# Performance work log

Measured on AMD Instinct MI355X. Metric: run time of the kernel, lower is better.

## Reference

```python
import jax, jax.numpy as jnp
import numpy as np

B, T, D, H = 64, 512, 1024, 1024

def setup_inputs() -> dict:
    key = jax.random.key(0)
    ks = jax.random.split(key, 7)
    s = 1.0 / np.sqrt(H).astype(np.float32)
    return {
        "x": jax.random.normal(ks[0], (B, T, D), jnp.float32),
        "hidden_state": jax.random.normal(ks[1], (1, B, H), jnp.float32),
        "dones": jax.random.randint(ks[2], (B, T), 0, 2, jnp.int32),
        "W_ih": jax.random.normal(ks[3], (3 * H, D), jnp.float32) * s,
        "W_hh": jax.random.normal(ks[4], (3 * H, H), jnp.float32) * s,
        "b_ih": jax.random.normal(ks[5], (3 * H,), jnp.float32) * s,
        "b_hh": jax.random.normal(ks[6], (3 * H,), jnp.float32) * s,
    }

def _resetting_gru(x, h0, dones, W_ih, W_hh, b_ih, b_hh):
    # x: [B,T,D], h0: [1,B,H], dones: [B,T]
    # Precompute input projection once: [B,T,3H] -> time-major [T,B,3H]
    gi = jnp.einsum('btd,gd->btg', x, W_ih) + b_ih
    gi = jnp.swapaxes(gi, 0, 1)
    # mask[t,b] = 0 where done==1 (hidden zeroed before consuming step t)
    mask = (1.0 - dones.astype(x.dtype)).T[:, :, None]  # [T,B,1]

    def step(h, inp):
        gi_t, m_t = inp          # [B,3H], [B,1]
        h = h * m_t              # inline reset at done timesteps
        gh = h @ W_hh.T + b_hh   # [B,3H]
        ir, iz, in_ = jnp.split(gi_t, 3, axis=-1)
        hr, hz, hn = jnp.split(gh, 3, axis=-1)
        r = jax.nn.sigmoid(ir + hr)
        z = jax.nn.sigmoid(iz + hz)
        n = jnp.tanh(in_ + r * hn)
        h_new = (1.0 - z) * n + z * h
        return h_new, h_new

    h_last, outs = jax.lax.scan(step, h0[0], (gi, mask))
    return jnp.swapaxes(outs, 0, 1), h_last[None]  # [B,T,H], [1,B,H]

def reference(x, hidden_state, dones, W_ih, W_hh, b_ih, b_hh):
    return _resetting_gru(x, hidden_state, dones, W_ih, W_hh, b_ih, b_hh)
```

## Files before the change

### kernel.cpp

```cpp
#include <hip/hip_runtime.h>
#include <hip/hip_cooperative_groups.h>

typedef short s16x8 __attribute__((ext_vector_type(8)));
typedef float f32x4 __attribute__((ext_vector_type(4)));
typedef float f32x2 __attribute__((ext_vector_type(2)));
typedef unsigned int u32x4 __attribute__((ext_vector_type(4)));
typedef unsigned int u32x2 __attribute__((ext_vector_type(2)));

#define B_ 64
#define T_ 512
#define D_ 1024
#define H_ 1024
#define TC_ 128

__device__ __forceinline__ unsigned short f2bf(float f) {
  union { float f; unsigned int u; } v; v.f = f;
  unsigned int r = v.u + 0x7fffu + ((v.u >> 16) & 1u);
  return (unsigned short)(r >> 16);
}
__device__ __forceinline__ float bf2f(unsigned short h) {
  union { unsigned int u; float f; } v; v.u = ((unsigned int)h) << 16;
  return v.f;
}

__device__ __forceinline__ void g2l16(const unsigned short* g, unsigned short* l) {
  __builtin_amdgcn_global_load_lds((const __attribute__((address_space(1))) unsigned int*)g,
                                   (__attribute__((address_space(3))) unsigned int*)l, 16, 0, 0);
}

__device__ __forceinline__ int haddr(int b, int k) {
  return (((b >> 4) * 32 + (k >> 5)) << 9) + ((b & 15) << 5) + (k & 31);
}

__global__ __launch_bounds__(256) void k_cvt_w(const float* __restrict__ w1, unsigned short* __restrict__ o1,
                                               const float* __restrict__ w2, unsigned short* __restrict__ o2) {
  int i = (blockIdx.x * 256 + threadIdx.x) * 4;
  float4 a = *(const float4*)(w1 + i);
  u32x2 p;
  p.x = (unsigned)f2bf(a.x) | ((unsigned)f2bf(a.y) << 16);
  p.y = (unsigned)f2bf(a.z) | ((unsigned)f2bf(a.w) << 16);
  *(u32x2*)(o1 + i) = p;
  float4 b = *(const float4*)(w2 + i);
  u32x2 q;
  q.x = (unsigned)f2bf(b.x) | ((unsigned)f2bf(b.y) << 16);
  q.y = (unsigned)f2bf(b.z) | ((unsigned)f2bf(b.w) << 16);
  *(u32x2*)(o2 + i) = q;
}

__global__ __launch_bounds__(256) void k_xt(const float* __restrict__ x, unsigned short* __restrict__ xt, int t0) {
  int m = blockIdx.x;
  int t = t0 + (m >> 6), b = m & 63;
  const float* src = x + ((size_t)(b * T_ + t)) * D_;
  unsigned short* dst = xt + (size_t)m * D_;
  int d = threadIdx.x * 4;
  float4 a = *(const float4*)(src + d);
  u32x2 p;
  p.x = (unsigned)f2bf(a.x) | ((unsigned)f2bf(a.y) << 16);
  p.y = (unsigned)f2bf(a.z) | ((unsigned)f2bf(a.w) << 16);
  *(u32x2*)(dst + d) = p;
}

__global__ __launch_bounds__(256) void k_misc(const float* __restrict__ h0, const int* __restrict__ dones,
                                              unsigned short* __restrict__ hb16T, float* __restrict__ hchk,
                                              float* __restrict__ maskT, unsigned int* __restrict__ bar,
                                              unsigned int* __restrict__ flag) {
  int i = blockIdx.x * 256 + threadIdx.x;
  int b = i >> 10, k = i & 1023;
  float v = h0[i];
  hchk[i] = v;
  int m0 = dones[b * T_];
  hb16T[haddr(b, k)] = m0 ? (unsigned short)0 : f2bf(v);
  if (i < T_ * B_) {
    int t = i >> 6, bb = i & 63;
    maskT[i] = dones[bb * T_ + t] ? 0.f : 1.f;
  }
  if (i == 0) { *bar = 0u; *flag = 0u; }
}

__global__ __launch_bounds__(256) void k_gemm(const unsigned short* __restrict__ A,
                                              const unsigned short* __restrict__ Bm,
                                              const float* __restrict__ bias,
                                              unsigned short* __restrict__ C) {
  __shared__ __align__(16) unsigned short As[128 * 40];
  __shared__ __align__(16) unsigned short Bs[128 * 40];
  const int tid = threadIdx.x;
  const int wave = tid >> 6, lane = tid & 63;
  const int q = lane >> 4, r = lane & 15;
  const int wm = wave >> 1, wn = wave & 1;
  const long m0 = (long)blockIdx.y * 128, n0 = (long)blockIdx.x * 128;
  f32x4 acc[4][4] = {};
  for (int k0 = 0; k0 < 1024; k0 += 32) {
    __syncthreads();
#pragma unroll
    for (int c0 = 0; c0 < 2; ++c0) {
      int c = c0 * 256 + tid;
      int row = c >> 2, kof = (c & 3) * 8;
      *(u32x4*)&As[row * 40 + kof] = *(const u32x4*)(A + (m0 + row) * 1024 + k0 + kof);
      *(u32x4*)&Bs[row * 40 + kof] = *(const u32x4*)(Bm + (n0 + row) * 1024 + k0 + kof);
    }
    __syncthreads();
    s16x8 af[4], bfr[4];
#pragma unroll
    for (int mt = 0; mt < 4; ++mt)
      af[mt] = *(const s16x8*)&As[(wm * 64 + mt * 16 + r) * 40 + q * 8];
#pragma unroll
    for (int nt = 0; nt < 4; ++nt)
      bfr[nt] = *(const s16x8*)&Bs[(wn * 64 + nt * 16 + r) * 40 + q * 8];
#pragma unroll
    for (int mt = 0; mt < 4; ++mt)
#pragma unroll
      for (int nt = 0; nt < 4; ++nt)
        acc[mt][nt] = __builtin_amdgcn_mfma_f32_16x16x32_bf16(af[mt], bfr[nt], acc[mt][nt], 0, 0, 0);
  }
#pragma unroll
  for (int nt = 0; nt < 4; ++nt) {
    long n = n0 + wn * 64 + nt * 16 + r;
    float bn = bias[n];
#pragma unroll
    for (int mt = 0; mt < 4; ++mt) {
#pragma unroll
      for (int reg = 0; reg < 4; ++reg) {
        long m = m0 + wm * 64 + mt * 16 + q * 4 + reg;
        C[m * 3072 + n] = f2bf(acc[mt][nt][reg] + bn);
      }
    }
  }
}

__global__ __launch_bounds__(512, 2) void k_gru(const unsigned short* __restrict__ whh,
                                                const float* __restrict__ bhh,
                                                const unsigned short* __restrict__ gi,
                                                const float* __restrict__ maskT,
                                                unsigned short* __restrict__ hb16T,
                                                float* __restrict__ hchk,
                                                float* __restrict__ out,
                                                unsigned int* __restrict__ bar,
                                                unsigned int* __restrict__ flag,
                                                int t0) {
  __shared__ __align__(16) unsigned char smem[131072];
  unsigned short* lds_h = (unsigned short*)smem;
  float* red = (float*)smem;
  const int tid = threadIdx.x;
  const int w = tid >> 6, lane = tid & 63;
  const int q = lane >> 4, r = lane & 15;
  const int j0 = blockIdx.x * 16;
  float* hlast = out + (size_t)B_ * T_ * H_;

  s16x8 Wreg[3][4];
#pragma unroll
  for (int g = 0; g < 3; ++g)
#pragma unroll
    for (int ks = 0; ks < 4; ++ks)
      Wreg[g][ks] = *(const s16x8*)(whh + ((size_t)(g * 1024 + j0 + r)) * 1024 + w * 128 + ks * 32 + q * 8);

  const int b0 = w * 8 + q * 2;
  const float bh0 = bhh[j0 + r];
  const float bh1 = bhh[1024 + j0 + r];
  const float bh2 = bhh[2048 + j0 + r];
  float hreg[2];
  hreg[0] = hchk[(size_t)b0 * 1024 + j0 + r];
  hreg[1] = hchk[(size_t)(b0 + 1) * 1024 + j0 + r];

  f32x4 acc[3][4] = {};
  float gcur[6], gnxt[6], mcur[2], mnxt[2], mncur[2], mnnxt[2];
#pragma unroll
  for (int e = 0; e < 2; ++e) {
    size_t mrow = (size_t)(b0 + e) * 3072;
    gcur[e * 3 + 0] = bf2f(gi[mrow + j0 + r]);
    gcur[e * 3 + 1] = bf2f(gi[mrow + 1024 + j0 + r]);
    gcur[e * 3 + 2] = bf2f(gi[mrow + 2048 + j0 + r]);
    mcur[e] = maskT[t0 * 64 + b0 + e];
    int tn = (t0 + 1 < 512) ? t0 + 1 : 511;
    mncur[e] = maskT[tn * 64 + b0 + e];
  }

  for (int tl = 0; tl < TC_; ++tl) {
    const int t = t0 + tl;
    const unsigned short* hsT = hb16T + (size_t)(t & 1) * 65536;
    unsigned short* hdT = hb16T + (size_t)((t + 1) & 1) * 65536;

    for (int c = w; c < 128; c += 8)
      g2l16(hsT + c * 512 + lane * 8, lds_h + c * 512);
    __syncthreads();

#pragma unroll
    for (int ks = 0; ks < 4; ++ks) {
      s16x8 a[4];
#pragma unroll
      for (int bt = 0; bt < 4; ++bt)
        a[bt] = *(const s16x8*)&lds_h[((bt * 32 + w * 4 + ks) << 9) + r * 32 + q * 8];
#pragma unroll
      for (int g = 0; g < 3; ++g)
#pragma unroll
        for (int bt = 0; bt < 4; ++bt)
          acc[g][bt] = __builtin_amdgcn_mfma_f32_16x16x32_bf16(a[bt], Wreg[g][ks], acc[g][bt], 0, 0, 0);
    }
    __syncthreads();

#pragma unroll
    for (int g = 0; g < 3; ++g)
#pragma unroll
      for (int bt = 0; bt < 4; ++bt) {
        *(f32x4*)&red[(size_t)((g * 8 + w) * 16 + r) * 68 + bt * 16 + q * 4] = acc[g][bt];
        acc[g][bt] = (f32x4){0.f, 0.f, 0.f, 0.f};
      }
    __syncthreads();

    f32x2 ps[3];
#pragma unroll
    for (int g = 0; g < 3; ++g) {
      f32x2 s = {0.f, 0.f};
#pragma unroll
      for (int kp = 0; kp < 8; ++kp)
        s += *(const f32x2*)&red[(size_t)((g * 8 + kp) * 16 + r) * 68 + b0];
      ps[g] = s;
    }
    float hn2[2];
#pragma unroll
    for (int e = 0; e < 2; ++e) {
      int b = b0 + e;
      float ghr = ps[0][e] + bh0;
      float ghz = ps[1][e] + bh1;
      float ghn = ps[2][e] + bh2;
      float rr = 1.f / (1.f + __expf(-(gcur[e * 3 + 0] + ghr)));
      float zz = 1.f / (1.f + __expf(-(gcur[e * 3 + 1] + ghz)));
      float nn = tanhf(gcur[e * 3 + 2] + rr * ghn);
      float hp = hreg[e] * mcur[e];
      float hn = (1.f - zz) * nn + zz * hp;
      hreg[e] = hn;
      hn2[e] = hn;
      unsigned short hv = (mncur[e] == 0.f) ? (unsigned short)0 : f2bf(hn);
      hdT[haddr(b, j0 + r)] = hv;
    }
    __syncthreads();

    if (tid == 0) {
      unsigned tgt = (unsigned)(t + 1);
      unsigned old = __hip_atomic_fetch_add(bar, 1u, __ATOMIC_RELEASE, __HIP_MEMORY_SCOPE_AGENT);
      if (old == 64u * tgt - 1u)
        __hip_atomic_store(flag, tgt, __ATOMIC_RELEASE, __HIP_MEMORY_SCOPE_AGENT);
    }

#pragma unroll
    for (int e = 0; e < 2; ++e) {
      int b = b0 + e;
      out[((size_t)b * 512 + t) * 1024 + j0 + r] = hn2[e];
      if (t == 511) hlast[(size_t)b * 1024 + j0 + r] = hn2[e];
      if (tl == TC_ - 1) hchk[(size_t)b * 1024 + j0 + r] = hn2[e];
    }
    if (tl + 1 < TC_) {
#pragma unroll
      for (int e = 0; e < 2; ++e) {
        size_t mrow = (size_t)((tl + 1) * 64 + b0 + e) * 3072;
        gnxt[e * 3 + 0] = bf2f(gi[mrow + j0 + r]);
        gnxt[e * 3 + 1] = bf2f(gi[mrow + 1024 + j0 + r]);
        gnxt[e * 3 + 2] = bf2f(gi[mrow + 2048 + j0 + r]);
        mnxt[e] = maskT[(t + 1) * 64 + b0 + e];
        int tn = (t + 2 < 512) ? t + 2 : 511;
        mnnxt[e] = maskT[tn * 64 + b0 + e];
      }
    }

    if (tid == 0) {
      while (__hip_atomic_load(flag, __ATOMIC_RELAXED, __HIP_MEMORY_SCOPE_AGENT) < (unsigned)(t + 1))
        __builtin_amdgcn_s_sleep(1);
      (void)__hip_atomic_load(bar, __ATOMIC_ACQUIRE, __HIP_MEMORY_SCOPE_AGENT);
    }
    __syncthreads();

#pragma unroll
    for (int e = 0; e < 2; ++e) {
      gcur[e * 3 + 0] = gnxt[e * 3 + 0];
      gcur[e * 3 + 1] = gnxt[e * 3 + 1];
      gcur[e * 3 + 2] = gnxt[e * 3 + 2];
      mcur[e] = mnxt[e];
      mncur[e] = mnnxt[e];
    }
  }
}

extern "C" void kernel_launch(void* const* d_in, const int* in_sizes, int n_in,
                              void* d_out, int out_size, void* d_ws, size_t ws_size,
                              hipStream_t stream) {
  const float* x     = (const float*)d_in[0];
  const float* h0    = (const float*)d_in[1];
  const int*   dones = (const int*)d_in[2];
  const float* Wih   = (const float*)d_in[3];
  const float* Whh   = (const float*)d_in[4];
  const float* bih   = (const float*)d_in[5];
  const float* bhh   = (const float*)d_in[6];
  float* out = (float*)d_out;
  char* ws = (char*)d_ws;
  unsigned short* wih_b = (unsigned short*)(ws);
  unsigned short* whh_b = (unsigned short*)(ws + 6291456);
  unsigned short* xt_c  = (unsigned short*)(ws + 12582912);
  unsigned short* gi_c  = (unsigned short*)(ws + 29360128);
  float*          maskT = (float*)(ws + 79691776);
  unsigned short* hb16T = (unsigned short*)(ws + 79822848);
  float*          hchk  = (float*)(ws + 80085248);
  unsigned int*   bar   = (unsigned int*)(ws + 80347392);
  unsigned int*   flag  = (unsigned int*)(ws + 80347520);

  k_cvt_w<<<3072, 256, 0, stream>>>(Wih, wih_b, Whh, whh_b);
  k_misc<<<256, 256, 0, stream>>>(h0, dones, hb16T, hchk, maskT, bar, flag);

  for (int c = 0; c < 4; ++c) {
    int t0 = c * TC_;
    k_xt<<<TC_ * 64, 256, 0, stream>>>(x, xt_c, t0);
    k_gemm<<<dim3(24, TC_ * 64 / 128), 256, 0, stream>>>(xt_c, wih_b, bih, gi_c);
    void* args[] = {(void*)&whh_b, (void*)&bhh, (void*)&gi_c, (void*)&maskT,
                    (void*)&hb16T, (void*)&hchk, (void*)&out, (void*)&bar, (void*)&flag, (void*)&t0};
    hipLaunchCooperativeKernel((const void*)k_gru, dim3(64), dim3(512), args, 0, stream);
  }
}
```

Measured before the change: 4.558 ms.

## Replace grid barrier with per-group counters and direct global h loads into registers

Replaces the single global atomic barrier/flag with eight per-group counters, so each wave waits only on the eight blocks that produce the hidden-state slice it reads. The hidden state moves to a plain row-major layout, and each wave loads its A fragments straight from global memory with cache-bypassing loads instead of staging them through LDS. This removes one full grid barrier and two block syncs per step and lets blocks proceed as soon as their dependencies are ready. The cost is more scattered global loads per wave, and correctness now depends on the group-counter ordering and on the uncached load semantics.

```diff
diff --git a/kernel.cpp b/kernel.cpp
--- a/kernel.cpp
+++ b/kernel.cpp
@@ -21,15 +21,6 @@
 __device__ __forceinline__ float bf2f(unsigned short h) {
   union { unsigned int u; float f; } v; v.u = ((unsigned int)h) << 16;
   return v.f;
-}
-
-__device__ __forceinline__ void g2l16(const unsigned short* g, unsigned short* l) {
-  __builtin_amdgcn_global_load_lds((const __attribute__((address_space(1))) unsigned int*)g,
-                                   (__attribute__((address_space(3))) unsigned int*)l, 16, 0, 0);
-}
-
-__device__ __forceinline__ int haddr(int b, int k) {
-  return (((b >> 4) * 32 + (k >> 5)) << 9) + ((b & 15) << 5) + (k & 31);
 }
 
 __global__ __launch_bounds__(256) void k_cvt_w(const float* __restrict__ w1, unsigned short* __restrict__ o1,
@@ -61,20 +52,19 @@
 }
 
 __global__ __launch_bounds__(256) void k_misc(const float* __restrict__ h0, const int* __restrict__ dones,
-                                              unsigned short* __restrict__ hb16T, float* __restrict__ hchk,
-                                              float* __restrict__ maskT, unsigned int* __restrict__ bar,
-                                              unsigned int* __restrict__ flag) {
+                                              unsigned short* __restrict__ hb16, float* __restrict__ hchk,
+                                              float* __restrict__ maskT, unsigned int* __restrict__ grp) {
   int i = blockIdx.x * 256 + threadIdx.x;
-  int b = i >> 10, k = i & 1023;
+  int b = i >> 10;
   float v = h0[i];
   hchk[i] = v;
   int m0 = dones[b * T_];
-  hb16T[haddr(b, k)] = m0 ? (unsigned short)0 : f2bf(v);
+  hb16[i] = m0 ? (unsigned short)0 : f2bf(v);
   if (i < T_ * B_) {
     int t = i >> 6, bb = i & 63;
     maskT[i] = dones[bb * T_ + t] ? 0.f : 1.f;
   }
-  if (i == 0) { *bar = 0u; *flag = 0u; }
+  if (i < 8) grp[i * 64] = 0u;
 }
 
 __global__ __launch_bounds__(256) void k_gemm(const unsigned short* __restrict__ A,
@@ -127,19 +117,16 @@
   }
 }
 
-__global__ __launch_bounds__(512, 2) void k_gru(const unsigned short* __restrict__ whh,
-                                                const float* __restrict__ bhh,
-                                                const unsigned short* __restrict__ gi,
-                                                const float* __restrict__ maskT,
-                                                unsigned short* __restrict__ hb16T,
-                                                float* __restrict__ hchk,
-                                                float* __restrict__ out,
-                                                unsigned int* __restrict__ bar,
-                                                unsigned int* __restrict__ flag,
-                                                int t0) {
-  __shared__ __align__(16) unsigned char smem[131072];
-  unsigned short* lds_h = (unsigned short*)smem;
-  float* red = (float*)smem;
+__global__ __launch_bounds__(512) void k_gru(const unsigned short* __restrict__ whh,
+                                             const float* __restrict__ bhh,
+                                             const unsigned short* __restrict__ gi,
+                                             const float* __restrict__ maskT,
+                                             unsigned short* __restrict__ hb16,
+                                             float* __restrict__ hchk,
+                                             float* __restrict__ out,
+                                             unsigned int* __restrict__ grp,
+                                             int t0) {
+  __shared__ __align__(16) float red[3 * 8 * 16 * 68];
   const int tid = threadIdx.x;
   const int w = tid >> 6, lane = tid & 63;
   const int q = lane >> 4, r = lane & 15;
@@ -160,6 +147,14 @@
   float hreg[2];
   hreg[0] = hchk[(size_t)b0 * 1024 + j0 + r];
   hreg[1] = hchk[(size_t)(b0 + 1) * 1024 + j0 + r];
+
+  unsigned rowoff[4];
+#pragma unroll
+  for (int bt = 0; bt < 4; ++bt)
+    rowoff[bt] = (unsigned)((bt * 16 + r) * 2048 + w * 256 + q * 16);
+
+  unsigned int* gw = grp + w * 64;
+  unsigned int* gmine = grp + (blockIdx.x >> 3) * 64;
 
   f32x4 acc[3][4] = {};
   float gcur[6], gnxt[6], mcur[2], mnxt[2], mncur[2], mnnxt[2];
@@ -176,26 +171,38 @@
 
   for (int tl = 0; tl < TC_; ++tl) {
     const int t = t0 + tl;
-    const unsigned short* hsT = hb16T + (size_t)(t & 1) * 65536;
-    unsigned short* hdT = hb16T + (size_t)((t + 1) & 1) * 65536;
-
-    for (int c = w; c < 128; c += 8)
-      g2l16(hsT + c * 512 + lane * 8, lds_h + c * 512);
-    __syncthreads();
-
-#pragma unroll
-    for (int ks = 0; ks < 4; ++ks) {
-      s16x8 a[4];
-#pragma unroll
-      for (int bt = 0; bt < 4; ++bt)
-        a[bt] = *(const s16x8*)&lds_h[((bt * 32 + w * 4 + ks) << 9) + r * 32 + q * 8];
+    const unsigned long long hs64 = (unsigned long long)(hb16 + (size_t)(t & 1) * 65536);
+    unsigned short* hd = hb16 + (size_t)((t + 1) & 1) * 65536;
+
+    {
+      const unsigned tgt = 8u * (unsigned)t;
+      while (__hip_atomic_load(gw, __ATOMIC_RELAXED, __HIP_MEMORY_SCOPE_AGENT) < tgt)
+        __builtin_amdgcn_s_sleep(1);
+    }
+
+    s16x8 fa[4][4];
+#pragma unroll
+    for (int bt = 0; bt < 4; ++bt) {
+      unsigned long long av = hs64 + rowoff[bt];
+      asm volatile("global_load_dwordx4 %0, %1, off sc0 sc1"
+                   : "=&v"(fa[bt][0]) : "v"(av) : "memory");
+      asm volatile("global_load_dwordx4 %0, %1, off offset:64 sc0 sc1"
+                   : "=&v"(fa[bt][1]) : "v"(av) : "memory");
+      asm volatile("global_load_dwordx4 %0, %1, off offset:128 sc0 sc1"
+                   : "=&v"(fa[bt][2]) : "v"(av) : "memory");
+      asm volatile("global_load_dwordx4 %0, %1, off offset:192 sc0 sc1"
+                   : "=&v"(fa[bt][3]) : "v"(av) : "memory");
+    }
+    asm volatile("s_waitcnt vmcnt(0)" ::: "memory");
+    __builtin_amdgcn_sched_barrier(0);
+
+#pragma unroll
+    for (int ks = 0; ks < 4; ++ks)
 #pragma unroll
       for (int g = 0; g < 3; ++g)
 #pragma unroll
         for (int bt = 0; bt < 4; ++bt)
-          acc[g][bt] = __builtin_amdgcn_mfma_f32_16x16x32_bf16(a[bt], Wreg[g][ks], acc[g][bt], 0, 0, 0);
-    }
-    __syncthreads();
+          acc[g][bt] = __builtin_amdgcn_mfma_f32_16x16x32_bf16(fa[bt][ks], Wreg[g][ks], acc[g][bt], 0, 0, 0);
 
 #pragma unroll
     for (int g = 0; g < 3; ++g)
@@ -218,7 +225,6 @@
     float hn2[2];
 #pragma unroll
     for (int e = 0; e < 2; ++e) {
-      int b = b0 + e;
       float ghr = ps[0][e] + bh0;
       float ghz = ps[1][e] + bh1;
       float ghn = ps[2][e] + bh2;
@@ -230,16 +236,12 @@
       hreg[e] = hn;
       hn2[e] = hn;
       unsigned short hv = (mncur[e] == 0.f) ? (unsigned short)0 : f2bf(hn);
-      hdT[haddr(b, j0 + r)] = hv;
+      hd[(size_t)(b0 + e) * 1024 + j0 + r] = hv;
     }
     __syncthreads();
 
-    if (tid == 0) {
-      unsigned tgt = (unsigned)(t + 1);
-      unsigned old = __hip_atomic_fetch_add(bar, 1u, __ATOMIC_RELEASE, __HIP_MEMORY_SCOPE_AGENT);
-      if (old == 64u * tgt - 1u)
-        __hip_atomic_store(flag, tgt, __ATOMIC_RELEASE, __HIP_MEMORY_SCOPE_AGENT);
-    }
+    if (tid == 0)
+      __hip_atomic_fetch_add(gmine, 1u, __ATOMIC_RELEASE, __HIP_MEMORY_SCOPE_AGENT);
 
 #pragma unroll
     for (int e = 0; e < 2; ++e) {
@@ -259,22 +261,14 @@
         int tn = (t + 2 < 512) ? t + 2 : 511;
         mnnxt[e] = maskT[tn * 64 + b0 + e];
       }
-    }
-
-    if (tid == 0) {
-      while (__hip_atomic_load(flag, __ATOMIC_RELAXED, __HIP_MEMORY_SCOPE_AGENT) < (unsigned)(t + 1))
-        __builtin_amdgcn_s_sleep(1);
-      (void)__hip_atomic_load(bar, __ATOMIC_ACQUIRE, __HIP_MEMORY_SCOPE_AGENT);
-    }
-    __syncthreads();
-
-#pragma unroll
-    for (int e = 0; e < 2; ++e) {
-      gcur[e * 3 + 0] = gnxt[e * 3 + 0];
-      gcur[e * 3 + 1] = gnxt[e * 3 + 1];
-      gcur[e * 3 + 2] = gnxt[e * 3 + 2];
-      mcur[e] = mnxt[e];
-      mncur[e] = mnnxt[e];
+#pragma unroll
+      for (int e = 0; e < 2; ++e) {
+        gcur[e * 3 + 0] = gnxt[e * 3 + 0];
+        gcur[e * 3 + 1] = gnxt[e * 3 + 1];
+        gcur[e * 3 + 2] = gnxt[e * 3 + 2];
+        mcur[e] = mnxt[e];
+        mncur[e] = mnnxt[e];
+      }
     }
   }
 }
@@ -296,20 +290,19 @@
   unsigned short* xt_c  = (unsigned short*)(ws + 12582912);
   unsigned short* gi_c  = (unsigned short*)(ws + 29360128);
   float*          maskT = (float*)(ws + 79691776);
-  unsigned short* hb16T = (unsigned short*)(ws + 79822848);
+  unsigned short* hb16  = (unsigned short*)(ws + 79822848);
   float*          hchk  = (float*)(ws + 80085248);
-  unsigned int*   bar   = (unsigned int*)(ws + 80347392);
-  unsigned int*   flag  = (unsigned int*)(ws + 80347520);
+  unsigned int*   grp   = (unsigned int*)(ws + 80347392);
 
   k_cvt_w<<<3072, 256, 0, stream>>>(Wih, wih_b, Whh, whh_b);
-  k_misc<<<256, 256, 0, stream>>>(h0, dones, hb16T, hchk, maskT, bar, flag);
+  k_misc<<<256, 256, 0, stream>>>(h0, dones, hb16, hchk, maskT, grp);
 
   for (int c = 0; c < 4; ++c) {
     int t0 = c * TC_;
     k_xt<<<TC_ * 64, 256, 0, stream>>>(x, xt_c, t0);
     k_gemm<<<dim3(24, TC_ * 64 / 128), 256, 0, stream>>>(xt_c, wih_b, bih, gi_c);
     void* args[] = {(void*)&whh_b, (void*)&bhh, (void*)&gi_c, (void*)&maskT,
-                    (void*)&hb16T, (void*)&hchk, (void*)&out, (void*)&bar, (void*)&flag, (void*)&t0};
+                    (void*)&hb16, (void*)&hchk, (void*)&out, (void*)&grp, (void*)&t0};
     hipLaunchCooperativeKernel((const void*)k_gru, dim3(64), dim3(512), args, 0, stream);
   }
 }
```

Result: slower. 4.912 ms (+7.8%).
